# Kernel optimization log

Measured on AMD Instinct MI355X. Metric: run time of the kernel, lower is better.

Reference implementation:

```python
import jax, jax.numpy as jnp
import numpy as np

V, D, H, L, T, B = 32000, 512, 8, 4, 2048, 2
HS = D // H


def setup_inputs() -> dict:
    key = jax.random.key(0)
    ks = jax.random.split(key, 10)
    s = 0.02  # init std, per _init_weights
    rn = lambda k, shape: jax.random.normal(k, shape, jnp.float32) * s
    return {
        "idx": jax.random.randint(ks[0], (B, T), 0, V),
        "tok_emb": rn(ks[1], (V, D)),
        "pos_emb": rn(ks[2], (T, D)),
        "ln1_g": jnp.ones((L, D)), "ln1_b": jnp.zeros((L, D)),
        "wq": rn(ks[3], (L, D, D)), "wk": rn(ks[4], (L, D, D)), "wv": rn(ks[5], (L, D, D)),
        "wo": rn(ks[6], (L, D, D)), "bo": jnp.zeros((L, D)),
        "ln2_g": jnp.ones((L, D)), "ln2_b": jnp.zeros((L, D)),
        "w1": rn(ks[7], (L, D, 4 * D)), "b1": jnp.zeros((L, 4 * D)),
        "w2": rn(ks[8], (L, 4 * D, D)), "b2": jnp.zeros((L, D)),
        "lnf_g": jnp.ones((D,)), "lnf_b": jnp.zeros((D,)),
        "head_w": rn(ks[9], (D, V)), "head_b": jnp.zeros((V,)),
    }


def _ln(x, g, b):
    mu = x.mean(-1, keepdims=True)
    var = ((x - mu) ** 2).mean(-1, keepdims=True)
    return (x - mu) * jax.lax.rsqrt(var + 1e-5) * g + b


def reference(idx, tok_emb, pos_emb, ln1_g, ln1_b, wq, wk, wv, wo, bo,
              ln2_g, ln2_b, w1, b1, w2, b2, lnf_g, lnf_b, head_w, head_b):
    Bb, Tt = idx.shape
    x = tok_emb[idx] + pos_emb[jnp.arange(Tt)]  # [B,T,D]
    mask = jnp.tril(jnp.ones((Tt, Tt), bool))
    scale = HS ** -0.5

    def block(x, p):
        g1, bb1, Wq, Wk, Wv, Wo, Bo, g2, bb2, W1, B1, W2, B2 = p
        h = _ln(x, g1, bb1)
        q = (h @ Wq).reshape(Bb, Tt, H, HS)
        k = (h @ Wk).reshape(Bb, Tt, H, HS)
        v = (h @ Wv).reshape(Bb, Tt, H, HS)
        wei = jnp.einsum('bthd,bshd->bhts', q, k) * scale  # [B,H,T,T]
        wei = jnp.where(mask, wei, -jnp.inf)
        wei = jax.nn.softmax(wei, axis=-1)
        att = jnp.einsum('bhts,bshd->bthd', wei, v).reshape(Bb, Tt, D)
        x = x + att @ Wo + Bo
        h2 = _ln(x, g2, bb2)
        x = x + jax.nn.relu(h2 @ W1 + B1) @ W2 + B2
        return x, None

    x, _ = jax.lax.scan(block, x, (ln1_g, ln1_b, wq, wk, wv, wo, bo,
                                   ln2_g, ln2_b, w1, b1, w2, b2))
    logits = _ln(x, lnf_g, lnf_b) @ head_w + head_b  # [B,T,V]
    return logits
```

## Files before the change

### kernel.cpp

```cpp
#include <hip/hip_runtime.h>
#include <hip/hip_bf16.h>
#include <cstddef>

typedef __bf16 bf16;
typedef __attribute__((ext_vector_type(8))) __bf16 bf16x8;
typedef __attribute__((ext_vector_type(4))) __bf16 bf16x4;
typedef __attribute__((ext_vector_type(4))) float f32x4;

constexpr int VOC = 32000;
constexpr int DIM = 512;
constexpr int NH  = 8;
constexpr int HSZ = 64;
constexpr int SEQ = 2048;
constexpr int NB  = 2;
constexpr int NL  = 4;
constexpr int NTOK = NB * SEQ;
constexpr int QS  = 3 * DIM;
constexpr int QKS = 2 * DIM;

__device__ __forceinline__ void gload16(const void* g, void* lds) {
  __builtin_amdgcn_global_load_lds(
      (const __attribute__((address_space(1))) unsigned int*)g,
      (__attribute__((address_space(3))) unsigned int*)lds, 16, 0, 0);
}

__global__ __launch_bounds__(256) void embed_kernel(
    const int* __restrict__ idx, const float* __restrict__ tok,
    const float* __restrict__ pos, float* __restrict__ x) {
  int i = blockIdx.x * 256 + threadIdx.x;
  int row = i >> 9;
  int d = i & (DIM - 1);
  int t = row & (SEQ - 1);
  int tk = idx[row];
  x[i] = tok[(size_t)tk * DIM + d] + pos[(size_t)t * DIM + d];
}

__global__ __launch_bounds__(256) void wt_all(
    const float* __restrict__ wq, const float* __restrict__ wk,
    const float* __restrict__ wv, const float* __restrict__ wo,
    const float* __restrict__ w1, const float* __restrict__ w2,
    const float* __restrict__ hw,
    bf16* __restrict__ wqkvT, bf16* __restrict__ woT,
    bf16* __restrict__ w1T, bf16* __restrict__ w2T, bf16* __restrict__ headT) {
  __shared__ float t[32][33];
  int bid = blockIdx.x;
  const float* src; bf16* dst; int K, N, n0, k0;
  if (bid < 12288) {
    int l = bid / 3072, tt = bid - l * 3072;
    if (tt < 1024) {
      int which = tt >> 8, u = tt & 255;
      K = DIM; N = DIM;
      n0 = (u & 15) * 32; k0 = (u >> 4) * 32;
      if (which == 0)      { src = wq + (size_t)l * DIM * DIM; dst = wqkvT + (size_t)l * QS * DIM; }
      else if (which == 1) { src = wk + (size_t)l * DIM * DIM; dst = wqkvT + (size_t)l * QS * DIM + DIM * DIM; }
      else if (which == 2) { src = wv + (size_t)l * DIM * DIM; dst = wqkvT + (size_t)l * QS * DIM + 2 * DIM * DIM; }
      else                 { src = wo + (size_t)l * DIM * DIM; dst = woT + (size_t)l * DIM * DIM; }
    } else if (tt < 2048) {
      int u = tt - 1024;
      K = DIM; N = 4 * DIM;
      n0 = (u & 63) * 32; k0 = (u >> 6) * 32;
      src = w1 + (size_t)l * DIM * 4 * DIM; dst = w1T + (size_t)l * 4 * DIM * DIM;
    } else {
      int u = tt - 2048;
      K = 4 * DIM; N = DIM;
      n0 = (u & 15) * 32; k0 = (u >> 4) * 32;
      src = w2 + (size_t)l * 4 * DIM * DIM; dst = w2T + (size_t)l * 4 * DIM * DIM;
    }
  } else {
    int u = bid - 12288;
    K = DIM; N = VOC;
    n0 = (u >> 4) * 32; k0 = (u & 15) * 32;
    src = hw; dst = headT;
  }
  int tx = threadIdx.x & 31, ty = threadIdx.x >> 5;
#pragma unroll
  for (int r = 0; r < 4; ++r)
    t[ty + r * 8][tx] = src[(size_t)(k0 + ty + r * 8) * N + n0 + tx];
  __syncthreads();
#pragma unroll
  for (int r = 0; r < 4; ++r)
    dst[(size_t)(n0 + ty + r * 8) * K + k0 + tx] = (bf16)t[tx][ty + r * 8];
}

__global__ __launch_bounds__(256) void ln_kernel(
    const float* __restrict__ x, const float* __restrict__ g,
    const float* __restrict__ b, bf16* __restrict__ out) {
  __shared__ float s1[4], s2[4];
  int row = blockIdx.x, tid = threadIdx.x;
  int lane = tid & 63, w = tid >> 6;
  const float* xr = x + (size_t)row * DIM;
  float a0 = xr[tid], a1 = xr[tid + 256];
  float ps = a0 + a1, pq = a0 * a0 + a1 * a1;
#pragma unroll
  for (int m = 1; m < 64; m <<= 1) {
    ps += __shfl_xor(ps, m, 64);
    pq += __shfl_xor(pq, m, 64);
  }
  if (lane == 0) { s1[w] = ps; s2[w] = pq; }
  __syncthreads();
  float fs = s1[0] + s1[1] + s1[2] + s1[3];
  float fq = s2[0] + s2[1] + s2[2] + s2[3];
  float mu = fs * (1.0f / DIM);
  float var = fq * (1.0f / DIM) - mu * mu;
  float rs = rsqrtf(var + 1e-5f);
  out[(size_t)row * DIM + tid] = (bf16)((a0 - mu) * rs * g[tid] + b[tid]);
  out[(size_t)row * DIM + tid + 256] =
      (bf16)((a1 - mu) * rs * g[tid + 256] + b[tid + 256]);
}

template <int BN, bool RELU, bool RES, bool OUTB, bool VSPLIT>
__global__ __launch_bounds__(256) void gemm128(
    const bf16* __restrict__ A, const bf16* __restrict__ Wt,
    const float* __restrict__ bias, const float* __restrict__ res,
    float* __restrict__ outF, bf16* __restrict__ outB, bf16* __restrict__ vTout,
    int K, int N, int ostride) {
  __shared__ bf16 As[128 * 64];
  __shared__ bf16 Bs[BN * 64];
  constexpr int WN = (BN == 128) ? 2 : 1;
  constexpr int WM = 4 / WN;
  constexpr int MP = 128 / WM / 16;
  constexpr int NP = BN / WN / 16;
  int tid = threadIdx.x;
  int wid = tid >> 6, ln = tid & 63;
  int lr = ln & 15, lg = ln >> 4;
  int bid = blockIdx.y * 32 + blockIdx.x;
  int cpx = gridDim.y * 4;
  int swz = (bid & 7) * cpx + (bid >> 3);
  int m0 = (swz & 31) * 128;
  int n0 = (swz >> 5) * BN;
  int wr = wid / WN, wc = wid % WN;
  f32x4 acc[MP][NP] = {};

  const char* Ab = (const char*)A;
  const char* Bb = (const char*)Wt;

  for (int k0 = 0; k0 < K; k0 += 64) {
    __syncthreads();
#pragma unroll
    for (int j = 0; j < 4; ++j) {
      int Lb = j * 4096 + wid * 1024;
      int L = Lb + ln * 16;
      int row = L >> 7;
      int colb = (L & 127) ^ ((row & 7) << 4);
      gload16(Ab + (size_t)(m0 + row) * (K * 2) + (size_t)k0 * 2 + colb,
              (char*)As + Lb);
    }
#pragma unroll
    for (int j = 0; j < BN / 32; ++j) {
      int Lb = j * 4096 + wid * 1024;
      int L = Lb + ln * 16;
      int row = L >> 7;
      int colb = (L & 127) ^ ((row & 7) << 4);
      gload16(Bb + (size_t)(n0 + row) * (K * 2) + (size_t)k0 * 2 + colb,
              (char*)Bs + Lb);
    }
    __syncthreads();
#pragma unroll
    for (int kk = 0; kk < 2; ++kk) {
      bf16x8 am[MP], bn[NP];
#pragma unroll
      for (int m = 0; m < MP; ++m) {
        int row = wr * (128 / WM) + m * 16 + lr;
        int cb = (kk * 64 + lg * 16) ^ ((row & 7) << 4);
        am[m] = *(const bf16x8*)((const char*)As + row * 128 + cb);
      }
#pragma unroll
      for (int n = 0; n < NP; ++n) {
        int row = wc * (BN / WN) + n * 16 + lr;
        int cb = (kk * 64 + lg * 16) ^ ((row & 7) << 4);
        bn[n] = *(const bf16x8*)((const char*)Bs + row * 128 + cb);
      }
#pragma unroll
      for (int m = 0; m < MP; ++m)
#pragma unroll
        for (int n = 0; n < NP; ++n)
          acc[m][n] = __builtin_amdgcn_mfma_f32_16x16x32_bf16(
              am[m], bn[n], acc[m][n], 0, 0, 0);
    }
  }

  if (VSPLIT && n0 >= 2 * DIM) {
#pragma unroll
    for (int m = 0; m < MP; ++m) {
      int mrow = m0 + wr * (128 / WM) + m * 16 + lg * 4;
      int bb = mrow >> 11, tt = mrow & (SEQ - 1);
#pragma unroll
      for (int n = 0; n < NP; ++n) {
        int d = n0 + wc * (BN / WN) + n * 16 + lr - 2 * DIM;
        bf16x4 pk;
#pragma unroll
        for (int i = 0; i < 4; ++i) pk[i] = (bf16)acc[m][n][i];
        *(bf16x4*)(vTout + ((size_t)(bb * NH + (d >> 6)) * HSZ + (d & 63)) * SEQ + tt) = pk;
      }
    }
    return;
  }

#pragma unroll
  for (int m = 0; m < MP; ++m) {
    int mrow = m0 + wr * (128 / WM) + m * 16 + lg * 4;
#pragma unroll
    for (int n = 0; n < NP; ++n) {
      int nc = n0 + wc * (BN / WN) + n * 16 + lr;
      float bval = bias ? bias[nc] : 0.0f;
#pragma unroll
      for (int i = 0; i < 4; ++i) {
        int mm = mrow + i;
        float val = acc[m][n][i] + bval;
        if (RELU) val = fmaxf(val, 0.0f);
        if (RES) val += res[(size_t)mm * ostride + nc];
        if (OUTB) outB[(size_t)mm * ostride + nc] = (bf16)val;
        else      outF[(size_t)mm * ostride + nc] = val;
      }
    }
  }
}

__global__ __launch_bounds__(256) void fattn_kernel(
    const bf16* __restrict__ qk, const bf16* __restrict__ vT,
    bf16* __restrict__ att) {
  __shared__ bf16 Ks[2][64 * 64];
  __shared__ bf16 Vs[2][64 * 64];
  __shared__ bf16 Pl[4][16][72];
  int tid = threadIdx.x;
  int wave = tid >> 6, lane = tid & 63;
  int lr = lane & 15, lg = lane >> 4;
  int h = blockIdx.y, b = blockIdx.z;
  int qt0 = ((b == 1) ? (gridDim.x - 1 - blockIdx.x) : blockIdx.x) * 64;
  const bf16* qb = qk + ((size_t)b * SEQ) * QKS + h * HSZ;
  const char* kb = (const char*)(qb + DIM);
  const char* vb = (const char*)(vT + (size_t)(b * NH + h) * HSZ * SEQ);

  bf16x8 aq[2];
  {
    const bf16* qr = qb + (size_t)(qt0 + wave * 16 + lr) * QKS + lg * 8;
    aq[0] = *(const bf16x8*)qr;
    aq[1] = *(const bf16x8*)(qr + 32);
  }

  f32x4 accO[4] = {};
  float m_r[4] = {-1e30f, -1e30f, -1e30f, -1e30f};
  float l_r[4] = {0.f, 0.f, 0.f, 0.f};

  int ntile = qt0 / 64 + 1;
#define STAGE(ti, buf)                                                        \
  {                                                                           \
    _Pragma("unroll")                                                         \
    for (int j = 0; j < 2; ++j) {                                             \
      int Lb = j * 4096 + wave * 1024;                                        \
      int L = Lb + lane * 16;                                                 \
      int row = L >> 7;                                                       \
      int cb = (L & 127) ^ ((row & 7) << 4);                                  \
      gload16(kb + (size_t)((ti) * 64 + row) * (QKS * 2) + cb,                \
              (char*)Ks[buf] + Lb);                                           \
      gload16(vb + (size_t)row * (SEQ * 2) + (ti) * 128 + cb,                 \
              (char*)Vs[buf] + Lb);                                           \
    }                                                                         \
  }

  STAGE(0, 0);
  int cur = 0;
  for (int ti = 0; ti < ntile; ++ti) {
    if (ti + 1 < ntile) {
      STAGE(ti + 1, cur ^ 1);
      asm volatile("s_waitcnt vmcnt(4)" ::: "memory");
    } else {
      asm volatile("s_waitcnt vmcnt(0)" ::: "memory");
    }
    __builtin_amdgcn_s_barrier();
    int kv0 = ti * 64;
    bool diag = (ti == ntile - 1);

    f32x4 sc[4];
#pragma unroll
    for (int s = 0; s < 4; ++s) {
      int row = s * 16 + lr;
      const char* base = (const char*)Ks[cur] + row * 128;
      bf16x8 b0 = *(const bf16x8*)(base + ((lg * 16) ^ ((row & 7) << 4)));
      bf16x8 b1 = *(const bf16x8*)(base + ((64 + lg * 16) ^ ((row & 7) << 4)));
      f32x4 z = {};
      z = __builtin_amdgcn_mfma_f32_16x16x32_bf16(aq[0], b0, z, 0, 0, 0);
      sc[s] = __builtin_amdgcn_mfma_f32_16x16x32_bf16(aq[1], b1, z, 0, 0, 0);
    }

#pragma unroll
    for (int i = 0; i < 4; ++i) {
      if (diag) {
        int qrow = qt0 + wave * 16 + lg * 4 + i;
#pragma unroll
        for (int s = 0; s < 4; ++s) {
          int kvc = kv0 + s * 16 + lr;
          sc[s][i] = (kvc <= qrow) ? sc[s][i] * 0.125f : -1e30f;
        }
      } else {
#pragma unroll
        for (int s = 0; s < 4; ++s) sc[s][i] *= 0.125f;
      }
      float t = fmaxf(fmaxf(sc[0][i], sc[1][i]), fmaxf(sc[2][i], sc[3][i]));
      t = fmaxf(t, __shfl_xor(t, 1, 64));
      t = fmaxf(t, __shfl_xor(t, 2, 64));
      t = fmaxf(t, __shfl_xor(t, 4, 64));
      t = fmaxf(t, __shfl_xor(t, 8, 64));
      if (t > m_r[i] + 8.0f) {
        float alpha = __expf(m_r[i] - t);
        m_r[i] = t;
        l_r[i] *= alpha;
#pragma unroll
        for (int ds = 0; ds < 4; ++ds) accO[ds][i] *= alpha;
      }
      float mm = m_r[i];
      float rs = 0.f;
#pragma unroll
      for (int s = 0; s < 4; ++s) {
        float p = __expf(sc[s][i] - mm);
        sc[s][i] = p;
        rs += p;
      }
      rs += __shfl_xor(rs, 1, 64);
      rs += __shfl_xor(rs, 2, 64);
      rs += __shfl_xor(rs, 4, 64);
      rs += __shfl_xor(rs, 8, 64);
      l_r[i] += rs;
    }

#pragma unroll
    for (int i = 0; i < 4; ++i)
#pragma unroll
      for (int s = 0; s < 4; ++s)
        Pl[wave][lg * 4 + i][s * 16 + lr] = (bf16)sc[s][i];
    bf16x8 pa0 = *(const bf16x8*)&Pl[wave][lr][lg * 8];
    bf16x8 pa1 = *(const bf16x8*)&Pl[wave][lr][32 + lg * 8];

#pragma unroll
    for (int ds = 0; ds < 4; ++ds) {
      int row = ds * 16 + lr;
      const char* base = (const char*)Vs[cur] + row * 128;
      bf16x8 v0 = *(const bf16x8*)(base + ((lg * 16) ^ ((row & 7) << 4)));
      bf16x8 v1 = *(const bf16x8*)(base + ((64 + lg * 16) ^ ((row & 7) << 4)));
      accO[ds] = __builtin_amdgcn_mfma_f32_16x16x32_bf16(pa0, v0, accO[ds], 0, 0, 0);
      accO[ds] = __builtin_amdgcn_mfma_f32_16x16x32_bf16(pa1, v1, accO[ds], 0, 0, 0);
    }
    __builtin_amdgcn_s_barrier();
    cur ^= 1;
  }
#undef STAGE

#pragma unroll
  for (int i = 0; i < 4; ++i) {
    float inv = 1.0f / l_r[i];
    size_t orow = ((size_t)b * SEQ + qt0 + wave * 16 + lg * 4 + i) * DIM + h * HSZ;
#pragma unroll
    for (int ds = 0; ds < 4; ++ds)
      att[orow + ds * 16 + lr] = (bf16)(accO[ds][i] * inv);
  }
}

extern "C" void kernel_launch(void* const* d_in, const int* in_sizes, int n_in,
                              void* d_out, int out_size, void* d_ws, size_t ws_size,
                              hipStream_t stream) {
  const int*   idx    = (const int*)d_in[0];
  const float* tok    = (const float*)d_in[1];
  const float* pos    = (const float*)d_in[2];
  const float* ln1_g  = (const float*)d_in[3];
  const float* ln1_b  = (const float*)d_in[4];
  const float* wq     = (const float*)d_in[5];
  const float* wk     = (const float*)d_in[6];
  const float* wv     = (const float*)d_in[7];
  const float* wo     = (const float*)d_in[8];
  const float* bo     = (const float*)d_in[9];
  const float* ln2_g  = (const float*)d_in[10];
  const float* ln2_b  = (const float*)d_in[11];
  const float* w1     = (const float*)d_in[12];
  const float* b1     = (const float*)d_in[13];
  const float* w2     = (const float*)d_in[14];
  const float* b2     = (const float*)d_in[15];
  const float* lnf_g  = (const float*)d_in[16];
  const float* lnf_b  = (const float*)d_in[17];
  const float* head_w = (const float*)d_in[18];
  const float* head_b = (const float*)d_in[19];

  char* W = (char*)d_ws;
  float* x     = (float*)(W);
  bf16*  h     = (bf16*)(W + 8388608);
  bf16*  qk    = (bf16*)(W + 12582912);
  bf16*  vTb   = (bf16*)(W + 20971520);
  bf16*  attb  = (bf16*)(W + 25165824);
  bf16*  ffn   = (bf16*)(W + 29360128);
  bf16*  wqkvT = (bf16*)(W + 46137344);
  bf16*  woT   = (bf16*)(W + 52428800);
  bf16*  w1T   = (bf16*)(W + 54525952);
  bf16*  w2T   = (bf16*)(W + 62914560);
  bf16*  headT = (bf16*)(W + 71303168);

  wt_all<<<12288 + 16000, 256, 0, stream>>>(wq, wk, wv, wo, w1, w2, head_w,
                                            wqkvT, woT, w1T, w2T, headT);
  embed_kernel<<<NTOK * DIM / 256, 256, 0, stream>>>(idx, tok, pos, x);

  dim3 gQKV(NTOK / 128, QS / 128);
  dim3 gD64(NTOK / 128, DIM / 64);
  dim3 gF(NTOK / 128, 4 * DIM / 128);
  dim3 gV(NTOK / 128, VOC / 128);
  dim3 gA(SEQ / 64, NH, NB);

  for (int l = 0; l < NL; ++l) {
    ln_kernel<<<NTOK, 256, 0, stream>>>(x, ln1_g + l * DIM, ln1_b + l * DIM, h);
    gemm128<128, false, false, true, true><<<gQKV, 256, 0, stream>>>(
        h, wqkvT + (size_t)l * QS * DIM, nullptr, nullptr, nullptr, qk, vTb,
        DIM, QS, QKS);
    fattn_kernel<<<gA, 256, 0, stream>>>(qk, vTb, attb);
    gemm128<64, false, true, false, false><<<gD64, 256, 0, stream>>>(
        attb, woT + (size_t)l * DIM * DIM, bo + l * DIM, x, x, nullptr, nullptr,
        DIM, DIM, DIM);
    ln_kernel<<<NTOK, 256, 0, stream>>>(x, ln2_g + l * DIM, ln2_b + l * DIM, h);
    gemm128<128, true, false, true, false><<<gF, 256, 0, stream>>>(
        h, w1T + (size_t)l * 4 * DIM * DIM, b1 + (size_t)l * 4 * DIM, nullptr,
        nullptr, ffn, nullptr, DIM, 4 * DIM, 4 * DIM);
    gemm128<64, false, true, false, false><<<gD64, 256, 0, stream>>>(
        ffn, w2T + (size_t)l * 4 * DIM * DIM, b2 + l * DIM, x, x, nullptr,
        nullptr, 4 * DIM, DIM, DIM);
  }

  ln_kernel<<<NTOK, 256, 0, stream>>>(x, lnf_g, lnf_b, h);
  gemm128<128, false, false, false, false><<<gV, 256, 0, stream>>>(
      h, headT, head_b, nullptr, (float*)d_out, nullptr, nullptr, DIM, VOC, VOC);
}
```

Baseline: 961.7 us.

## Double-buffer GEMM loads, widen attention to 128-row tiles, fuse embed with LN

The GEMM mainloop gains a second LDS buffer so the next K-tile's global-to-LDS loads are issued before computing on the current one, with vmcnt waits and barriers replacing the two syncthreads. The attention kernel now runs 512 threads covering 128 query rows per block, which halves the number of blocks and shares each K/V tile across more waves; causal masking is now decided per wave. The embedding lookup is fused with the first layer's LayerNorm to save one kernel launch and one pass over x. In exchange, LDS use rises and the attention grid gets smaller, which may hurt occupancy and load balance.

New measurement: 1.055 ms. 9.7% more time.

```diff
diff --git a/kernel.cpp b/kernel.cpp
--- a/kernel.cpp
+++ b/kernel.cpp
@@ -22,17 +22,6 @@
   __builtin_amdgcn_global_load_lds(
       (const __attribute__((address_space(1))) unsigned int*)g,
       (__attribute__((address_space(3))) unsigned int*)lds, 16, 0, 0);
-}
-
-__global__ __launch_bounds__(256) void embed_kernel(
-    const int* __restrict__ idx, const float* __restrict__ tok,
-    const float* __restrict__ pos, float* __restrict__ x) {
-  int i = blockIdx.x * 256 + threadIdx.x;
-  int row = i >> 9;
-  int d = i & (DIM - 1);
-  int t = row & (SEQ - 1);
-  int tk = idx[row];
-  x[i] = tok[(size_t)tk * DIM + d] + pos[(size_t)t * DIM + d];
 }
 
 __global__ __launch_bounds__(256) void wt_all(
@@ -82,6 +71,37 @@
     dst[(size_t)(n0 + ty + r * 8) * K + k0 + tx] = (bf16)t[tx][ty + r * 8];
 }
 
+__global__ __launch_bounds__(256) void emln_kernel(
+    const int* __restrict__ idx, const float* __restrict__ tok,
+    const float* __restrict__ pos, const float* __restrict__ g,
+    const float* __restrict__ b, float* __restrict__ x, bf16* __restrict__ h) {
+  __shared__ float s1[4], s2[4];
+  int row = blockIdx.x, tid = threadIdx.x;
+  int lane = tid & 63, w = tid >> 6;
+  int t = row & (SEQ - 1);
+  int tk = idx[row];
+  float a0 = tok[(size_t)tk * DIM + tid] + pos[(size_t)t * DIM + tid];
+  float a1 = tok[(size_t)tk * DIM + tid + 256] + pos[(size_t)t * DIM + tid + 256];
+  x[(size_t)row * DIM + tid] = a0;
+  x[(size_t)row * DIM + tid + 256] = a1;
+  float ps = a0 + a1, pq = a0 * a0 + a1 * a1;
+#pragma unroll
+  for (int m = 1; m < 64; m <<= 1) {
+    ps += __shfl_xor(ps, m, 64);
+    pq += __shfl_xor(pq, m, 64);
+  }
+  if (lane == 0) { s1[w] = ps; s2[w] = pq; }
+  __syncthreads();
+  float fs = s1[0] + s1[1] + s1[2] + s1[3];
+  float fq = s2[0] + s2[1] + s2[2] + s2[3];
+  float mu = fs * (1.0f / DIM);
+  float var = fq * (1.0f / DIM) - mu * mu;
+  float rs = rsqrtf(var + 1e-5f);
+  h[(size_t)row * DIM + tid] = (bf16)((a0 - mu) * rs * g[tid] + b[tid]);
+  h[(size_t)row * DIM + tid + 256] =
+      (bf16)((a1 - mu) * rs * g[tid + 256] + b[tid + 256]);
+}
+
 __global__ __launch_bounds__(256) void ln_kernel(
     const float* __restrict__ x, const float* __restrict__ g,
     const float* __restrict__ b, bf16* __restrict__ out) {
@@ -114,8 +134,8 @@
     const float* __restrict__ bias, const float* __restrict__ res,
     float* __restrict__ outF, bf16* __restrict__ outB, bf16* __restrict__ vTout,
     int K, int N, int ostride) {
-  __shared__ bf16 As[128 * 64];
-  __shared__ bf16 Bs[BN * 64];
+  __shared__ bf16 As[2][128 * 64];
+  __shared__ bf16 Bs[2][BN * 64];
   constexpr int WN = (BN == 128) ? 2 : 1;
   constexpr int WM = 4 / WN;
   constexpr int MP = 128 / WM / 16;
@@ -134,27 +154,41 @@
   const char* Ab = (const char*)A;
   const char* Bb = (const char*)Wt;
 
+#define GSTAGE(k0s, buf)                                                      \
+  {                                                                           \
+    _Pragma("unroll")                                                         \
+    for (int j = 0; j < 4; ++j) {                                             \
+      int Lb = j * 4096 + wid * 1024;                                         \
+      int L = Lb + ln * 16;                                                   \
+      int row = L >> 7;                                                       \
+      int colb = (L & 127) ^ ((row & 7) << 4);                                \
+      gload16(Ab + (size_t)(m0 + row) * (K * 2) + (size_t)(k0s) * 2 + colb,   \
+              (char*)As[buf] + Lb);                                           \
+    }                                                                         \
+    _Pragma("unroll")                                                         \
+    for (int j = 0; j < BN / 32; ++j) {                                       \
+      int Lb = j * 4096 + wid * 1024;                                         \
+      int L = Lb + ln * 16;                                                   \
+      int row = L >> 7;                                                       \
+      int colb = (L & 127) ^ ((row & 7) << 4);                                \
+      gload16(Bb + (size_t)(n0 + row) * (K * 2) + (size_t)(k0s) * 2 + colb,   \
+              (char*)Bs[buf] + Lb);                                           \
+    }                                                                         \
+  }
+
+  GSTAGE(0, 0);
+  int cur = 0;
   for (int k0 = 0; k0 < K; k0 += 64) {
-    __syncthreads();
-#pragma unroll
-    for (int j = 0; j < 4; ++j) {
-      int Lb = j * 4096 + wid * 1024;
-      int L = Lb + ln * 16;
-      int row = L >> 7;
-      int colb = (L & 127) ^ ((row & 7) << 4);
-      gload16(Ab + (size_t)(m0 + row) * (K * 2) + (size_t)k0 * 2 + colb,
-              (char*)As + Lb);
-    }
-#pragma unroll
-    for (int j = 0; j < BN / 32; ++j) {
-      int Lb = j * 4096 + wid * 1024;
-      int L = Lb + ln * 16;
-      int row = L >> 7;
-      int colb = (L & 127) ^ ((row & 7) << 4);
-      gload16(Bb + (size_t)(n0 + row) * (K * 2) + (size_t)k0 * 2 + colb,
-              (char*)Bs + Lb);
-    }
-    __syncthreads();
+    if (k0 + 64 < K) {
+      GSTAGE(k0 + 64, cur ^ 1);
+      if constexpr (BN == 128)
+        asm volatile("s_waitcnt vmcnt(8)" ::: "memory");
+      else
+        asm volatile("s_waitcnt vmcnt(6)" ::: "memory");
+    } else {
+      asm volatile("s_waitcnt vmcnt(0)" ::: "memory");
+    }
+    __builtin_amdgcn_s_barrier();
 #pragma unroll
     for (int kk = 0; kk < 2; ++kk) {
       bf16x8 am[MP], bn[NP];
@@ -162,13 +196,13 @@
       for (int m = 0; m < MP; ++m) {
         int row = wr * (128 / WM) + m * 16 + lr;
         int cb = (kk * 64 + lg * 16) ^ ((row & 7) << 4);
-        am[m] = *(const bf16x8*)((const char*)As + row * 128 + cb);
+        am[m] = *(const bf16x8*)((const char*)As[cur] + row * 128 + cb);
       }
 #pragma unroll
       for (int n = 0; n < NP; ++n) {
         int row = wc * (BN / WN) + n * 16 + lr;
         int cb = (kk * 64 + lg * 16) ^ ((row & 7) << 4);
-        bn[n] = *(const bf16x8*)((const char*)Bs + row * 128 + cb);
+        bn[n] = *(const bf16x8*)((const char*)Bs[cur] + row * 128 + cb);
       }
 #pragma unroll
       for (int m = 0; m < MP; ++m)
@@ -177,7 +211,10 @@
           acc[m][n] = __builtin_amdgcn_mfma_f32_16x16x32_bf16(
               am[m], bn[n], acc[m][n], 0, 0, 0);
     }
-  }
+    __builtin_amdgcn_s_barrier();
+    cur ^= 1;
+  }
+#undef GSTAGE
 
   if (VSPLIT && n0 >= 2 * DIM) {
 #pragma unroll
@@ -216,17 +253,17 @@
   }
 }
 
-__global__ __launch_bounds__(256) void fattn_kernel(
+__global__ __launch_bounds__(512) void fattn_kernel(
     const bf16* __restrict__ qk, const bf16* __restrict__ vT,
     bf16* __restrict__ att) {
   __shared__ bf16 Ks[2][64 * 64];
   __shared__ bf16 Vs[2][64 * 64];
-  __shared__ bf16 Pl[4][16][72];
+  __shared__ bf16 Pl[8][16][72];
   int tid = threadIdx.x;
   int wave = tid >> 6, lane = tid & 63;
   int lr = lane & 15, lg = lane >> 4;
   int h = blockIdx.y, b = blockIdx.z;
-  int qt0 = ((b == 1) ? (gridDim.x - 1 - blockIdx.x) : blockIdx.x) * 64;
+  int qt0 = ((b == 1) ? (gridDim.x - 1 - blockIdx.x) : blockIdx.x) * 128;
   const bf16* qb = qk + ((size_t)b * SEQ) * QKS + h * HSZ;
   const char* kb = (const char*)(qb + DIM);
   const char* vb = (const char*)(vT + (size_t)(b * NH + h) * HSZ * SEQ);
@@ -242,20 +279,16 @@
   float m_r[4] = {-1e30f, -1e30f, -1e30f, -1e30f};
   float l_r[4] = {0.f, 0.f, 0.f, 0.f};
 
-  int ntile = qt0 / 64 + 1;
+  int ntile = qt0 / 64 + 2;
 #define STAGE(ti, buf)                                                        \
   {                                                                           \
-    _Pragma("unroll")                                                         \
-    for (int j = 0; j < 2; ++j) {                                             \
-      int Lb = j * 4096 + wave * 1024;                                        \
-      int L = Lb + lane * 16;                                                 \
-      int row = L >> 7;                                                       \
-      int cb = (L & 127) ^ ((row & 7) << 4);                                  \
-      gload16(kb + (size_t)((ti) * 64 + row) * (QKS * 2) + cb,                \
-              (char*)Ks[buf] + Lb);                                           \
-      gload16(vb + (size_t)row * (SEQ * 2) + (ti) * 128 + cb,                 \
-              (char*)Vs[buf] + Lb);                                           \
-    }                                                                         \
+    int L = wave * 1024 + lane * 16;                                          \
+    int row = L >> 7;                                                         \
+    int cb = (L & 127) ^ ((row & 7) << 4);                                    \
+    gload16(kb + (size_t)((ti) * 64 + row) * (QKS * 2) + cb,                  \
+            (char*)Ks[buf] + wave * 1024);                                    \
+    gload16(vb + (size_t)row * (SEQ * 2) + (ti) * 128 + cb,                   \
+            (char*)Vs[buf] + wave * 1024);                                    \
   }
 
   STAGE(0, 0);
@@ -263,13 +296,13 @@
   for (int ti = 0; ti < ntile; ++ti) {
     if (ti + 1 < ntile) {
       STAGE(ti + 1, cur ^ 1);
-      asm volatile("s_waitcnt vmcnt(4)" ::: "memory");
+      asm volatile("s_waitcnt vmcnt(2)" ::: "memory");
     } else {
       asm volatile("s_waitcnt vmcnt(0)" ::: "memory");
     }
     __builtin_amdgcn_s_barrier();
     int kv0 = ti * 64;
-    bool diag = (ti == ntile - 1);
+    bool needmask = (kv0 + 63) > (qt0 + wave * 16);
 
     f32x4 sc[4];
 #pragma unroll
@@ -285,7 +318,7 @@
 
 #pragma unroll
     for (int i = 0; i < 4; ++i) {
-      if (diag) {
+      if (needmask) {
         int qrow = qt0 + wave * 16 + lg * 4 + i;
 #pragma unroll
         for (int s = 0; s < 4; ++s) {
@@ -394,20 +427,21 @@
 
   wt_all<<<12288 + 16000, 256, 0, stream>>>(wq, wk, wv, wo, w1, w2, head_w,
                                             wqkvT, woT, w1T, w2T, headT);
-  embed_kernel<<<NTOK * DIM / 256, 256, 0, stream>>>(idx, tok, pos, x);
+  emln_kernel<<<NTOK, 256, 0, stream>>>(idx, tok, pos, ln1_g, ln1_b, x, h);
 
   dim3 gQKV(NTOK / 128, QS / 128);
   dim3 gD64(NTOK / 128, DIM / 64);
   dim3 gF(NTOK / 128, 4 * DIM / 128);
   dim3 gV(NTOK / 128, VOC / 128);
-  dim3 gA(SEQ / 64, NH, NB);
+  dim3 gA(SEQ / 128, NH, NB);
 
   for (int l = 0; l < NL; ++l) {
-    ln_kernel<<<NTOK, 256, 0, stream>>>(x, ln1_g + l * DIM, ln1_b + l * DIM, h);
+    if (l > 0)
+      ln_kernel<<<NTOK, 256, 0, stream>>>(x, ln1_g + l * DIM, ln1_b + l * DIM, h);
     gemm128<128, false, false, true, true><<<gQKV, 256, 0, stream>>>(
         h, wqkvT + (size_t)l * QS * DIM, nullptr, nullptr, nullptr, qk, vTb,
         DIM, QS, QKS);
-    fattn_kernel<<<gA, 256, 0, stream>>>(qk, vTb, attb);
+    fattn_kernel<<<gA, 512, 0, stream>>>(qk, vTb, attb);
     gemm128<64, false, true, false, false><<<gD64, 256, 0, stream>>>(
         attb, woT + (size_t)l * DIM * DIM, bo + l * DIM, x, x, nullptr, nullptr,
         DIM, DIM, DIM);
```
